# Optimization experiments

Measured on AMD Instinct MI355X. Metric: run time of the kernel, lower is better.

The kernel has to match this reference:

```python
import jax, jax.numpy as jnp
import numpy as np

NCE_T = 0.07  # opt.nce_T
EPS = 1e-8    # torch CosineSimilarity eps

def setup_inputs() -> dict:
    key = jax.random.key(0)
    k1, k2, k3 = jax.random.split(key, 3)
    num_patches, C = 4096, 256
    features = jax.random.normal(k1, (2, num_patches, C), dtype=jnp.float32)
    labels_seg = jax.random.randint(k2, (1, 1, 128, 128, 128), 0, 5, dtype=jnp.int32)
    labels_coords = jax.random.randint(k3, (num_patches, 3), 0, 64, dtype=jnp.int32)
    return {"features": features, "labels_seg": labels_seg,
            "labels_coords": labels_coords, "cr_w": 64, "cr_h": 64, "cr_d": 64}

def _sup_nce_loss(features, lab):
    # features: (ntps, N, C); lab: (N,) int class per patch
    ntps, N, C = features.shape
    M = ntps * N
    f = features.reshape(M, C)
    nrm = jnp.linalg.norm(f, axis=-1)  # (M,)
    # cosine similarity = (f @ f^T) / max(|x||y|, eps), then / temperature
    sim = (f @ f.T) / jnp.maximum(nrm[:, None] * nrm[None, :], EPS)
    logits = sim / NCE_T
    logits = logits - jax.lax.stop_gradient(jnp.max(logits, axis=1, keepdims=True))
    pos = (lab[:, None] == lab[None, :]).astype(f.dtype)        # (N,N)
    pos = jnp.tile(pos, (ntps, ntps))                            # (M,M)
    diag_off = 1.0 - jnp.eye(M, dtype=f.dtype)                   # logits_mask
    pos = pos * diag_off
    denom = jnp.log((jnp.exp(logits) * diag_off).sum(1, keepdims=True))
    log_prob = logits - denom
    mean_log_prob_pos = (pos * log_prob).sum(1) / pos.sum(1)
    return -(mean_log_prob_pos.reshape(ntps, N)).mean()

def reference(features, labels_seg, labels_coords, cr_w, cr_h, cr_d):
    # nearest-neighbor downsample of labels to coords_range (torch 'nearest': floor(i*in/out))
    H, W, D = labels_seg.shape[2], labels_seg.shape[3], labels_seg.shape[4]
    iw = (jnp.arange(cr_w) * H) // cr_w
    ih = (jnp.arange(cr_h) * W) // cr_h
    idd = (jnp.arange(cr_d) * D) // cr_d
    seg = labels_seg[0, 0][iw][:, ih][:, :, idd]  # (cr_w, cr_h, cr_d)
    lab = seg[labels_coords[:, 0], labels_coords[:, 1], labels_coords[:, 2]]  # (N,)
    return _sup_nce_loss(features, lab)
```

## Files before the change

kernel.cpp:

```cpp
#include <hip/hip_runtime.h>
#include <hip/hip_bf16.h>

typedef __attribute__((ext_vector_type(4))) float floatx4;

#define C_DIM 256
#define INV_T 14.285714285714286f
#define K2_SCALE 20.60992915f

__device__ __forceinline__ unsigned int pack4fp8(float a, float b, float c, float d) {
    int w = __builtin_amdgcn_cvt_pk_fp8_f32(a, b, 0, false);
    w = __builtin_amdgcn_cvt_pk_fp8_f32(c, d, w, true);
    return (unsigned int)w;
}

template <int CTRL>
__device__ __forceinline__ float dppadd(float x) {
    int y = __builtin_amdgcn_update_dpp(0, __builtin_bit_cast(int, x),
                                        CTRL, 0xf, 0xf, true);
    return x + __builtin_bit_cast(float, y);
}
__device__ __forceinline__ float row16_sum(float x) {
    x = dppadd<0xB1>(x);
    x = dppadd<0x4E>(x);
    x = dppadd<0x124>(x);
    x = dppadd<0x128>(x);
    return x;
}

__device__ __forceinline__ void decode_tile(int idx, int nt, int& tm, int& tn) {
    float fnt = (float)nt;
    float disc = (2.0f * fnt + 1.0f) * (2.0f * fnt + 1.0f) - 8.0f * (float)idx;
    int t = (int)((2.0f * fnt + 1.0f - sqrtf(disc)) * 0.5f);
    if (t < 0) t = 0;
    if (t > nt - 1) t = nt - 1;
    while (t > 0 && idx < t * nt - t * (t - 1) / 2) --t;
    while (idx >= (t + 1) * nt - (t + 1) * t / 2) ++t;
    tm = t;
    tn = t + (idx - (t * nt - t * (t - 1) / 2));
}

__global__ __launch_bounds__(256) void
norm_kernel(const float* __restrict__ f,
            unsigned char* __restrict__ g2,
            const int* __restrict__ seg,
            const int* __restrict__ coords,
            const int* __restrict__ crw,
            const int* __restrict__ crh,
            const int* __restrict__ crd,
            int* __restrict__ lab,
            float* __restrict__ Spart,
            int* __restrict__ histpart,
            float* __restrict__ acc_done,
            int N, int H, int W, int D) {
    __shared__ float nrm[16][264];
    __shared__ float Sloc[5][256];
    __shared__ int lbl[16];
    __shared__ int histloc[8];

    const int tid = threadIdx.x;
    const int bid = blockIdx.x;
    const int lane = tid & 63;
    const int wave = tid >> 6;
    const int rbase = bid * 32;

    if (bid == 0 && tid == 0) {
        acc_done[0] = 0.0f;
        ((int*)acc_done)[1] = 0;
    }
    if (tid < 8) histloc[tid] = 0;
#pragma unroll
    for (int c = 0; c < 5; ++c) Sloc[c][tid] = 0.0f;
    __syncthreads();

    for (int g = 0; g < 2; ++g) {
        const int grow0 = rbase + g * 16;
        if (tid < 16) {
            const int row = grow0 + tid;
            const int p = row & (N - 1);
            int c0 = coords[3 * p + 0];
            int c1 = coords[3 * p + 1];
            int c2 = coords[3 * p + 2];
            int i0 = (c0 * H) / crw[0];
            int i1 = (c1 * W) / crh[0];
            int i2 = (c2 * D) / crd[0];
            const int c = seg[(i0 * W + i1) * D + i2];
            lbl[tid] = c;
            if (row < N) {
                lab[row] = c;
                atomicAdd(&histloc[c], 1);
            }
        }
        const int rl = wave * 4;
#pragma unroll
        for (int q = 0; q < 4; ++q) {
            const int row = grow0 + rl + q;
            const float4 v = ((const float4*)(f + (size_t)row * C_DIM))[lane];
            float ss = v.x * v.x + v.y * v.y + v.z * v.z + v.w * v.w;
#pragma unroll
            for (int off = 32; off; off >>= 1) ss += __shfl_xor(ss, off, 64);
            const float inv = 1.0f / sqrtf(ss);
            *(float4*)&nrm[rl + q][lane * 4] =
                float4{v.x * inv, v.y * inv, v.z * inv, v.w * inv};
        }
        __syncthreads();

        const int k0 = (tid >> 5) * 32 + ((tid >> 3) & 3) * 8;
        const float* ra = &nrm[(2 * tid) & 15][k0];
        const float* rb = &nrm[(2 * tid + 1) & 15][k0];
        uint4 o;
        o.x = pack4fp8(ra[0], ra[1], ra[2], ra[3]);
        o.y = pack4fp8(ra[4], ra[5], ra[6], ra[7]);
        o.z = pack4fp8(rb[0], rb[1], rb[2], rb[3]);
        o.w = pack4fp8(rb[4], rb[5], rb[6], rb[7]);
        *(uint4*)(g2 + (size_t)(bid * 2 + g) * 4096 + (size_t)tid * 16) = o;

#pragma unroll
        for (int rr = 0; rr < 16; ++rr)
            Sloc[lbl[rr]][tid] += nrm[rr][tid];
        __syncthreads();
    }

#pragma unroll
    for (int c = 0; c < 5; ++c)
        Spart[(size_t)bid * 1280 + c * 256 + tid] = Sloc[c][tid];
    if (tid < 8) histpart[bid * 8 + tid] = histloc[tid];
}

__global__ __launch_bounds__(256, 2) void
gram_kernel(const unsigned char* __restrict__ G2,
            float* __restrict__ part,
            int M, int nt) {
    __shared__ unsigned char Abuf[32768];
    __shared__ unsigned char Bbuf[32768];
    __shared__ float red[2][2][128];

    const int tid = threadIdx.x;
    const int bid = blockIdx.x;
    const int lane = tid & 63;
    const int wave = tid >> 6;
    const int waveM = wave >> 1;
    const int waveN = wave & 1;
    const int cc = lane & 15;
    const int cq = lane >> 4;

    const int start = bid * 4 + (bid < 32 ? bid : 32);
    const int len = 4 + (bid < 32 ? 1 : 0);

    int tmCur, tnCur;
    decode_tile(start, nt, tmCur, tnCur);

    {
        const unsigned char* gA = G2 + (size_t)tmCur * 32768;
#pragma unroll
        for (int i = 0; i < 8; ++i) {
            const int u = i * 256 + tid;
            __builtin_amdgcn_global_load_lds(
                (const __attribute__((address_space(1))) void*)(gA + (size_t)u * 16),
                (__attribute__((address_space(3))) void*)(&Abuf[(u & ~63) * 16]),
                16, 0, 0);
        }
        if (tnCur != tmCur) {
            const unsigned char* gB = G2 + (size_t)tnCur * 32768;
#pragma unroll
            for (int i = 0; i < 8; ++i) {
                const int u = i * 256 + tid;
                __builtin_amdgcn_global_load_lds(
                    (const __attribute__((address_space(1))) void*)(gB + (size_t)u * 16),
                    (__attribute__((address_space(3))) void*)(&Bbuf[(u & ~63) * 16]),
                    16, 0, 0);
            }
        }
    }

    for (int s = 0; s < len; ++s) {
        const int tm = tmCur, tn = tnCur;
        const int rowA0 = tm * 128;
        const int rowB0 = tn * 128;
        const bool diagTile = (tm == tn);
        const unsigned char* A = Abuf;
        const unsigned char* B = diagTile ? Abuf : Bbuf;

        __syncthreads();

        floatx4 acc[4][4];
#pragma unroll
        for (int mi = 0; mi < 4; ++mi)
#pragma unroll
            for (int ni = 0; ni < 4; ++ni)
                acc[mi][ni] = floatx4{-1.0f, -1.0f, -1.0f, -1.0f};

#pragma unroll
        for (int ks = 0; ks < 8; ++ks) {
            long af[4], bf[4];
#pragma unroll
            for (int mi = 0; mi < 4; ++mi)
                af[mi] = *(const long*)&A[(size_t)((waveM * 4 + mi) * 8 + ks) * 512 + lane * 8];
#pragma unroll
            for (int ni = 0; ni < 4; ++ni)
                bf[ni] = *(const long*)&B[(size_t)((waveN * 4 + ni) * 8 + ks) * 512 + lane * 8];
#pragma unroll
            for (int mi = 0; mi < 4; ++mi)
#pragma unroll
                for (int ni = 0; ni < 4; ++ni)
                    acc[mi][ni] = __builtin_amdgcn_mfma_f32_16x16x32_fp8_fp8(
                        af[mi], bf[ni], acc[mi][ni], 0, 0, 0);
        }

        __syncthreads();

        if (s + 1 < len) {
            int tmN, tnN;
            decode_tile(start + s + 1, nt, tmN, tnN);
            if (tmN != tm) {
                const unsigned char* gA = G2 + (size_t)tmN * 32768;
#pragma unroll
                for (int i = 0; i < 8; ++i) {
                    const int u = i * 256 + tid;
                    __builtin_amdgcn_global_load_lds(
                        (const __attribute__((address_space(1))) void*)(gA + (size_t)u * 16),
                        (__attribute__((address_space(3))) void*)(&Abuf[(u & ~63) * 16]),
                        16, 0, 0);
                }
            }
            if (tnN != tmN) {
                const unsigned char* gB = G2 + (size_t)tnN * 32768;
#pragma unroll
                for (int i = 0; i < 8; ++i) {
                    const int u = i * 256 + tid;
                    __builtin_amdgcn_global_load_lds(
                        (const __attribute__((address_space(1))) void*)(gB + (size_t)u * 16),
                        (__attribute__((address_space(3))) void*)(&Bbuf[(u & ~63) * 16]),
                        16, 0, 0);
                }
            }
            tmCur = tmN;
            tnCur = tnN;
        }

        if (!diagTile) {
            float bse[4] = {};
#pragma unroll
            for (int mi = 0; mi < 4; ++mi) {
#pragma unroll
                for (int r = 0; r < 4; ++r) {
                    const int lrow = waveM * 64 + mi * 16 + cq * 4 + r;
                    float se = 0.0f;
#pragma unroll
                    for (int ni = 0; ni < 4; ++ni) {
                        const float e = exp2f(acc[mi][ni][r] * K2_SCALE);
                        se += e;
                        bse[ni] += e;
                    }
                    se = row16_sum(se);
                    if (cc == 0) red[0][waveN][lrow] = se;
                }
            }
#pragma unroll
            for (int ni = 0; ni < 4; ++ni) {
                float se = bse[ni];
                se += __shfl_xor(se, 16, 64);
                se += __shfl_xor(se, 32, 64);
                if (cq == 0) red[1][waveM][waveN * 64 + ni * 16 + cc] = se;
            }
        } else {
#pragma unroll
            for (int mi = 0; mi < 4; ++mi) {
#pragma unroll
                for (int r = 0; r < 4; ++r) {
                    const int lrow = waveM * 64 + mi * 16 + cq * 4 + r;
                    const int grow = rowA0 + lrow;
                    float se = 0.0f;
#pragma unroll
                    for (int ni = 0; ni < 4; ++ni) {
                        const int gcol = rowB0 + waveN * 64 + ni * 16 + cc;
                        const float e = exp2f(acc[mi][ni][r] * K2_SCALE);
                        se += (gcol != grow) ? e : 0.0f;
                    }
                    se = row16_sum(se);
                    if (cc == 0) red[0][waveN][lrow] = se;
                }
            }
        }
        __syncthreads();

        if (tid < 128)
            part[(size_t)tn * M + rowA0 + tid] = red[0][0][tid] + red[0][1][tid];
        if (!diagTile && tid >= 128)
            part[(size_t)tm * M + rowB0 + (tid - 128)] =
                red[1][0][tid - 128] + red[1][1][tid - 128];
    }
}

__global__ __launch_bounds__(256) void
finalize_kernel(const float* __restrict__ part,
                const float* __restrict__ Spart,
                const int* __restrict__ histpart,
                float* __restrict__ acc_done,
                float* __restrict__ out,
                int M, int N, int nslots, int fblk) {
    __shared__ float sred[256];
    __shared__ int hred[256];

    const int tid = threadIdx.x;
    const int bid = blockIdx.x;
    const int ntps = M / N;
    const int nblk = fblk + 5;
    float blocksum = 0.0f;

    if (bid < fblk) {
        const int r0 = bid * 256;
        float se = 0.0f;
        for (int s = 0; s < nslots; ++s) se += part[(size_t)s * M + r0 + tid];
        sred[tid] = -logf(se);
        __syncthreads();
        for (int k = 128; k; k >>= 1) {
            if (tid < k) sred[tid] += sred[tid + k];
            __syncthreads();
        }
        blocksum = sred[0];
    } else {
        const int c = bid - fblk;
        float a0 = 0.0f, a1 = 0.0f, a2 = 0.0f, a3 = 0.0f;
        float a4 = 0.0f, a5 = 0.0f, a6 = 0.0f, a7 = 0.0f;
        const float* Sp = Spart + c * 256 + tid;
        for (int b = 0; b < 256; b += 8) {
            a0 += Sp[(size_t)(b + 0) * 1280];
            a1 += Sp[(size_t)(b + 1) * 1280];
            a2 += Sp[(size_t)(b + 2) * 1280];
            a3 += Sp[(size_t)(b + 3) * 1280];
            a4 += Sp[(size_t)(b + 4) * 1280];
            a5 += Sp[(size_t)(b + 5) * 1280];
            a6 += Sp[(size_t)(b + 6) * 1280];
            a7 += Sp[(size_t)(b + 7) * 1280];
        }
        const float v = ((a0 + a1) + (a2 + a3)) + ((a4 + a5) + (a6 + a7));
        sred[tid] = v * v;
        hred[tid] = histpart[tid * 8 + c];
        __syncthreads();
        for (int k = 128; k; k >>= 1) {
            if (tid < k) {
                sred[tid] += sred[tid + k];
                hred[tid] += hred[tid + k];
            }
            __syncthreads();
        }
        if (tid == 0) {
            const float S2 = sred[0];
            const float Mc = (float)(ntps * hred[0]);
            const float cnt = Mc - 1.0f;
            float contrib = (cnt > 0.0f) ? INV_T * (S2 - Mc) / cnt : 0.0f;
            if (c == 0) contrib -= INV_T * (float)M;
            blocksum = contrib;
        }
    }

    if (tid == 0) {
        atomicAdd(&acc_done[0], blocksum);
        __threadfence();
        int old = atomicAdd((int*)&acc_done[1], 1);
        if (old == nblk - 1) {
            float total = atomicAdd(&acc_done[0], 0.0f);
            out[0] = -total / (float)M;
        }
    }
}

extern "C" void kernel_launch(void* const* d_in, const int* in_sizes, int n_in,
                              void* d_out, int out_size, void* d_ws, size_t ws_size,
                              hipStream_t stream) {
    const float* features = (const float*)d_in[0];
    const int* labels_seg = (const int*)d_in[1];
    const int* labels_coords = (const int*)d_in[2];
    const int* crw = (const int*)d_in[3];
    const int* crh = (const int*)d_in[4];
    const int* crd = (const int*)d_in[5];
    float* out = (float*)d_out;

    const int N = in_sizes[2] / 3;
    const int M = in_sizes[0] / C_DIM;
    const int H = 128, W = 128, D = 128;
    const int nt = M / 128;

    char* ws = (char*)d_ws;
    unsigned char* g2 = (unsigned char*)ws;
    char* p1 = ws + (size_t)M * C_DIM;
    int* lab = (int*)p1;
    char* p2 = p1 + (size_t)N * 4;
    float* part = (float*)p2;
    char* p3 = p2 + (size_t)nt * M * 4;
    float* Spart = (float*)p3;
    char* p4 = p3 + (size_t)256 * 1280 * 4;
    int* histpart = (int*)p4;
    float* acc_done = (float*)(p4 + 256 * 8 * 4);

    norm_kernel<<<M / 32, 256, 0, stream>>>(features, g2, labels_seg,
                                            labels_coords, crw, crh, crd, lab,
                                            Spart, histpart, acc_done,
                                            N, H, W, D);

    gram_kernel<<<512, 256, 0, stream>>>(g2, part, M, nt);

    const int fblk = M / 256;
    finalize_kernel<<<fblk + 5, 256, 0, stream>>>(part, Spart, histpart,
                                                  acc_done, out, M, N, nt, fblk);
}
```

Baseline: 121.1 us.

## Fuse finalize reduction into gram kernel via grid-wide atomic barrier

```diff
diff --git a/kernel.cpp b/kernel.cpp
--- a/kernel.cpp
+++ b/kernel.cpp
@@ -66,6 +66,7 @@
     if (bid == 0 && tid == 0) {
         acc_done[0] = 0.0f;
         ((int*)acc_done)[1] = 0;
+        ((int*)acc_done)[2] = 0;
     }
     if (tid < 8) histloc[tid] = 0;
 #pragma unroll
@@ -129,7 +130,11 @@
 __global__ __launch_bounds__(256, 2) void
 gram_kernel(const unsigned char* __restrict__ G2,
             float* __restrict__ part,
-            int M, int nt) {
+            const float* __restrict__ Spart,
+            const int* __restrict__ histpart,
+            float* __restrict__ acc_done,
+            float* __restrict__ out,
+            int M, int N, int nt) {
     __shared__ unsigned char Abuf[32768];
     __shared__ unsigned char Bbuf[32768];
     __shared__ float red[2][2][128];
@@ -289,37 +294,58 @@
             part[(size_t)tm * M + rowB0 + (tid - 128)] =
                 red[1][0][tid - 128] + red[1][1][tid - 128];
     }
-}
-
-__global__ __launch_bounds__(256) void
-finalize_kernel(const float* __restrict__ part,
-                const float* __restrict__ Spart,
-                const int* __restrict__ histpart,
-                float* __restrict__ acc_done,
-                float* __restrict__ out,
-                int M, int N, int nslots, int fblk) {
-    __shared__ float sred[256];
-    __shared__ int hred[256];
-
-    const int tid = threadIdx.x;
-    const int bid = blockIdx.x;
-    const int ntps = M / N;
-    const int nblk = fblk + 5;
-    float blocksum = 0.0f;
-
-    if (bid < fblk) {
-        const int r0 = bid * 256;
+
+    __syncthreads();
+    int* ctr = (int*)acc_done + 2;
+    const int ntot = (int)gridDim.x;
+    if (tid == 0) {
+        __threadfence();
+        __hip_atomic_fetch_add(ctr, 1, __ATOMIC_RELEASE, __HIP_MEMORY_SCOPE_AGENT);
+    }
+
+    const int rowblks = M >> 5;
+    const int nblk = rowblks + 5;
+
+    if (bid < rowblks) {
+        if (tid == 0) {
+            while (__hip_atomic_load(ctr, __ATOMIC_RELAXED,
+                                     __HIP_MEMORY_SCOPE_AGENT) < ntot)
+                __builtin_amdgcn_s_sleep(2);
+        }
+        __syncthreads();
+        __threadfence();
+
+        float* tr = (float*)Abuf;
+        const int r_off = tid & 31;
+        const int s_hi = tid >> 5;
+        const int r0 = bid * 32;
         float se = 0.0f;
-        for (int s = 0; s < nslots; ++s) se += part[(size_t)s * M + r0 + tid];
-        sred[tid] = -logf(se);
-        __syncthreads();
-        for (int k = 128; k; k >>= 1) {
-            if (tid < k) sred[tid] += sred[tid + k];
-            __syncthreads();
-        }
-        blocksum = sred[0];
-    } else {
-        const int c = bid - fblk;
+#pragma unroll
+        for (int j = 0; j < 64; j += 8)
+            se += part[(size_t)(s_hi + j) * (size_t)M + r0 + r_off];
+        tr[tid] = se;
+        __syncthreads();
+
+        float bs = 0.0f;
+        if (tid < 32) {
+            float t = ((tr[tid] + tr[tid + 32]) + (tr[tid + 64] + tr[tid + 96])) +
+                      ((tr[tid + 128] + tr[tid + 160]) + (tr[tid + 192] + tr[tid + 224]));
+            float v = -logf(t);
+#pragma unroll
+            for (int off = 16; off; off >>= 1) v += __shfl_xor(v, off, 32);
+            bs = v;
+        }
+        if (tid == 0) {
+            atomicAdd(&acc_done[0], bs);
+            __threadfence();
+            int old = atomicAdd((int*)acc_done + 1, 1);
+            if (old == nblk - 1)
+                out[0] = -atomicAdd(&acc_done[0], 0.0f) / (float)M;
+        }
+    } else if (bid < rowblks + 5) {
+        const int c = bid - rowblks;
+        float* sred = (float*)Abuf;
+        int* hred = (int*)(Abuf + 4096);
         float a0 = 0.0f, a1 = 0.0f, a2 = 0.0f, a3 = 0.0f;
         float a4 = 0.0f, a5 = 0.0f, a6 = 0.0f, a7 = 0.0f;
         const float* Sp = Spart + c * 256 + tid;
@@ -345,22 +371,17 @@
             __syncthreads();
         }
         if (tid == 0) {
+            const int ntps = M / N;
             const float S2 = sred[0];
             const float Mc = (float)(ntps * hred[0]);
             const float cnt = Mc - 1.0f;
             float contrib = (cnt > 0.0f) ? INV_T * (S2 - Mc) / cnt : 0.0f;
             if (c == 0) contrib -= INV_T * (float)M;
-            blocksum = contrib;
-        }
-    }
-
-    if (tid == 0) {
-        atomicAdd(&acc_done[0], blocksum);
-        __threadfence();
-        int old = atomicAdd((int*)&acc_done[1], 1);
-        if (old == nblk - 1) {
-            float total = atomicAdd(&acc_done[0], 0.0f);
-            out[0] = -total / (float)M;
+            atomicAdd(&acc_done[0], contrib);
+            __threadfence();
+            int old = atomicAdd((int*)acc_done + 1, 1);
+            if (old == nblk - 1)
+                out[0] = -atomicAdd(&acc_done[0], 0.0f) / (float)M;
         }
     }
 }
@@ -398,9 +419,6 @@
                                             Spart, histpart, acc_done,
                                             N, H, W, D);
 
-    gram_kernel<<<512, 256, 0, stream>>>(g2, part, M, nt);
-
-    const int fblk = M / 256;
-    finalize_kernel<<<fblk + 5, 256, 0, stream>>>(part, Spart, histpart,
-                                                  acc_done, out, M, N, nt, fblk);
-}
+    gram_kernel<<<512, 256, 0, stream>>>(g2, part, Spart, histpart,
+                                         acc_done, out, M, N, nt);
+}
```

After: 168.2 us. 1.39x slower.
